# Kernel tuning notes

Measured on AMD Instinct MI355X. Metric: run time of the kernel, lower is better.

## Reference

```python
import jax, jax.numpy as jnp
import numpy as np

B, IN, OUT = 131072, 512, 512


def setup_inputs() -> dict:
    key = jax.random.key(0)
    k1, k2 = jax.random.split(key)
    x = jax.random.normal(k1, (B, IN), dtype=jnp.float32)
    # matches reset_parameters: normal(0, sqrt(1/in_features))
    weight = jax.random.normal(k2, (OUT, IN), dtype=jnp.float32) * jnp.sqrt(1.0 / IN)
    bias = jnp.zeros((OUT,), dtype=jnp.float32)
    return {"x": x, "weight": weight, "bias": bias}


def _binarize(w):
    # deterministic sign binarization: w >= 0 -> +1, else -1
    return jnp.where(w >= 0, 1.0, -1.0).astype(w.dtype)


def reference(x, weight, bias):
    wb = _binarize(weight)            # [out, in], values in {-1, +1}
    # out = x @ wb.T + bias           # [B, out]
    return jnp.einsum("bi,oi->bo", x, wb) + bias
```

## Files before the change

kernel.cpp:

```cpp
#include <hip/hip_runtime.h>
#include <stdint.h>


#define BATCH   131072
#define IN_F    512
#define OUT_F   512
#define BM      64
#define NCH     8
#define BUFB    16384

using f32x4  = __attribute__((ext_vector_type(4))) float;
using f32x16 = __attribute__((ext_vector_type(16))) float;
using short8 = __attribute__((ext_vector_type(8))) short;
using usv8   = __attribute__((ext_vector_type(8))) unsigned short;
using u32    = uint32_t;

__global__ void prep_w(const float* __restrict__ W, unsigned short* __restrict__ wf) {
    int t = blockIdx.x * blockDim.x + threadIdx.x;
    int l  = t & 63;
    int nf = (t >> 6) & 15;
    int kt = t >> 10;
    int n = nf * 32 + (l & 31);
    int k = kt * 16 + ((l >> 5) << 3);
    const float* src = W + (size_t)n * IN_F + k;
    f32x4 w0 = *(const f32x4*)(src);
    f32x4 w1 = *(const f32x4*)(src + 4);
    usv8 o;
#pragma unroll
    for (int j = 0; j < 4; ++j) {
        o[j]     = (w0[j] >= 0.0f) ? 0x3F80u : 0xBF80u;
        o[j + 4] = (w1[j] >= 0.0f) ? 0x3F80u : 0xBF80u;
    }
    *(usv8*)(wf + (size_t)t * 8) = o;
}

__global__ __launch_bounds__(512, 4) void gemm_bin(
    const float* __restrict__ X, const unsigned short* __restrict__ WF,
    const float* __restrict__ bias, float* __restrict__ out) {

    __shared__ __align__(16) char smem[4 * BUFB];

    const int tid  = threadIdx.x;
    const int lane = tid & 63;
    const int wv   = tid >> 6;
    const int m0   = blockIdx.x * BM;

    const int dr   = wv * 4 + (lane >> 4);
    const int ds4  = ((lane & 15) ^ (dr & 15)) << 2;
    const float* src0 = X + (size_t)(m0 + dr) * IN_F + ds4;
    const float* src1 = src0 + (size_t)32 * IN_F;

#define ISSUE_DMA(ck_)                                                         \
    {                                                                          \
        char* b_ = smem + ((ck_) & 3) * BUFB + wv * 1024;                      \
        __builtin_amdgcn_global_load_lds(                                      \
            (const __attribute__((address_space(1))) void*)(src0 + (ck_) * 64),\
            (__attribute__((address_space(3))) void*)(b_), 16, 0, 0);          \
        __builtin_amdgcn_global_load_lds(                                      \
            (const __attribute__((address_space(1))) void*)(src1 + (ck_) * 64),\
            (__attribute__((address_space(3))) void*)(b_ + 8192), 16, 0, 0);   \
    }

    const short8* wb = (const short8*)(WF) + ((size_t)(wv * 2) * 64 + lane);
#define LDB(dst, g_)                                                           \
    {                                                                          \
        _Pragma("unroll")                                                      \
        for (int fn = 0; fn < 2; ++fn)                                         \
            dst[fn] = wb[(g_) * 1024 + fn * 64];                               \
    }

    const int arow = (lane & 31) * 256;
    const int aq32 = (lane >> 5) << 5;
    const int aswz = (lane & 15) << 4;

#define LDA_CVT(dst, ab_, kt4_)                                                \
    {                                                                          \
        _Pragma("unroll")                                                      \
        for (int rg = 0; rg < 2; ++rg) {                                       \
            const char* p_  = (ab_) + rg * 8192 + arow;                        \
            const int  blo_ = (((kt4_) << 6) + aq32) ^ aswz;                   \
            f32x4 lo_ = *(const f32x4*)(p_ + blo_);                            \
            f32x4 hi_ = *(const f32x4*)(p_ + (blo_ ^ 16));                     \
            u32 w0_, w1_, w2_, w3_;                                            \
            asm("v_cvt_pk_bf16_f32 %0, %1, %2" : "=v"(w0_)                     \
                : "v"(lo_[0]), "v"(lo_[1]));                                   \
            asm("v_cvt_pk_bf16_f32 %0, %1, %2" : "=v"(w1_)                     \
                : "v"(lo_[2]), "v"(lo_[3]));                                   \
            asm("v_cvt_pk_bf16_f32 %0, %1, %2" : "=v"(w2_)                     \
                : "v"(hi_[0]), "v"(hi_[1]));                                   \
            asm("v_cvt_pk_bf16_f32 %0, %1, %2" : "=v"(w3_)                     \
                : "v"(hi_[2]), "v"(hi_[3]));                                   \
            union { u32 w[4]; short8 v; } pk_;                                 \
            pk_.w[0] = w0_; pk_.w[1] = w1_; pk_.w[2] = w2_; pk_.w[3] = w3_;    \
            dst[rg] = pk_.v;                                                   \
        }                                                                      \
    }

    f32x16 acc[2][2];
#pragma unroll
    for (int fn = 0; fn < 2; ++fn) {
        const float bv = bias[wv * 64 + fn * 32 + (lane & 31)];
#pragma unroll
        for (int rg = 0; rg < 2; ++rg)
#pragma unroll
            for (int r = 0; r < 16; ++r) acc[rg][fn][r] = bv;
    }

    ISSUE_DMA(0);
    ISSUE_DMA(1);

    short8 bf[2][2];
#pragma unroll
    for (int ck = 0; ck < NCH; ++ck) {
        LDB(bf[0], ck * 4 + 0);
        LDB(bf[1], ck * 4 + 1);
        __builtin_amdgcn_sched_barrier(0);
        if (ck < NCH - 1) asm volatile("s_waitcnt vmcnt(6)" ::: "memory");
        else              asm volatile("s_waitcnt vmcnt(4)" ::: "memory");
        __builtin_amdgcn_sched_barrier(0);
        __builtin_amdgcn_s_barrier();
        __builtin_amdgcn_sched_barrier(0);

        const char* ab = smem + (ck & 3) * BUFB;
        short8 af[2];
#pragma unroll
        for (int kt4 = 0; kt4 < 4; ++kt4) {
            LDA_CVT(af, ab, kt4);
            __builtin_amdgcn_s_setprio(1);
#pragma unroll
            for (int rg = 0; rg < 2; ++rg)
#pragma unroll
                for (int fn = 0; fn < 2; ++fn)
                    acc[rg][fn] = __builtin_amdgcn_mfma_f32_32x32x16_bf16(
                        af[rg], bf[kt4 & 1][fn], acc[rg][fn], 0, 0, 0);
            __builtin_amdgcn_s_setprio(0);
            if (kt4 < 2) LDB(bf[kt4 & 1], ck * 4 + kt4 + 2);
            if (kt4 == 1 && ck + 2 < NCH) {
                __builtin_amdgcn_sched_barrier(0);
                ISSUE_DMA(ck + 2);
                __builtin_amdgcn_sched_barrier(0);
            }
        }
    }
#undef ISSUE_DMA
#undef LDB
#undef LDA_CVT

    const int c     = lane & 31;
    const int rbase = (lane >> 5) << 2;
#pragma unroll
    for (int rg = 0; rg < 2; ++rg)
#pragma unroll
        for (int fn = 0; fn < 2; ++fn)
#pragma unroll
            for (int r = 0; r < 16; ++r) {
                const int row = rg * 32 + (r & 3) + 8 * (r >> 2) + rbase;
                out[(size_t)(m0 + row) * OUT_F + wv * 64 + fn * 32 + c] =
                    acc[rg][fn][r];
            }
}

extern "C" void kernel_launch(void* const* d_in, const int* in_sizes, int n_in,
                              void* d_out, int out_size, void* d_ws, size_t ws_size,
                              hipStream_t stream) {
    const float* X    = (const float*)d_in[0];
    const float* W    = (const float*)d_in[1];
    const float* bias = (const float*)d_in[2];
    float* o          = (float*)d_out;
    unsigned short* wf = (unsigned short*)d_ws;

    hipLaunchKernelGGL(prep_w, dim3(128), dim3(256), 0, stream, W, wf);
    hipLaunchKernelGGL(gemm_bin, dim3(BATCH / BM), dim3(512), 0, stream,
                       X, wf, bias, o);
}
```

Measured before the change: 138.8 us.

## Pack binarized weights into sign bits and split output columns across XCD-mapped blocks

```diff
diff --git a/kernel.cpp b/kernel.cpp
--- a/kernel.cpp
+++ b/kernel.cpp
@@ -5,37 +5,51 @@
 #define BATCH   131072
 #define IN_F    512
 #define OUT_F   512
-#define BM      64
+#define BM      32
 #define NCH     8
-#define BUFB    16384
+#define BUFB    8192
 
 using f32x4  = __attribute__((ext_vector_type(4))) float;
 using f32x16 = __attribute__((ext_vector_type(16))) float;
 using short8 = __attribute__((ext_vector_type(8))) short;
-using usv8   = __attribute__((ext_vector_type(8))) unsigned short;
 using u32    = uint32_t;
+using u64    = unsigned long long;
 
-__global__ void prep_w(const float* __restrict__ W, unsigned short* __restrict__ wf) {
+__global__ void prep_wbits(const float* __restrict__ W, u32* __restrict__ wp) {
     int t = blockIdx.x * blockDim.x + threadIdx.x;
     int l  = t & 63;
-    int nf = (t >> 6) & 15;
-    int kt = t >> 10;
-    int n = nf * 32 + (l & 31);
-    int k = kt * 16 + ((l >> 5) << 3);
-    const float* src = W + (size_t)n * IN_F + k;
-    f32x4 w0 = *(const f32x4*)(src);
-    f32x4 w1 = *(const f32x4*)(src + 4);
-    usv8 o;
+    int nf = t >> 6;
+    const float* row = W + (size_t)(nf * 32 + (l & 31)) * IN_F + ((l >> 5) << 3);
 #pragma unroll
-    for (int j = 0; j < 4; ++j) {
-        o[j]     = (w0[j] >= 0.0f) ? 0x3F80u : 0xBF80u;
-        o[j + 4] = (w1[j] >= 0.0f) ? 0x3F80u : 0xBF80u;
+    for (int q = 0; q < 8; ++q) {
+        u32 word = 0;
+#pragma unroll
+        for (int b = 0; b < 4; ++b) {
+            const float* p = row + (q * 4 + b) * 16;
+            u32 by = 0;
+#pragma unroll
+            for (int j = 0; j < 8; ++j)
+                by |= (p[j] >= 0.0f ? 0u : 1u) << j;
+            word |= by << (8 * b);
+        }
+        wp[(size_t)t * 8 + q] = word;
     }
-    *(usv8*)(wf + (size_t)t * 8) = o;
 }
 
-__global__ __launch_bounds__(512, 4) void gemm_bin(
-    const float* __restrict__ X, const unsigned short* __restrict__ WF,
+__device__ __forceinline__ short8 expB(u32 bb) {
+    const u64 MUL = 0x1000200040008000ull;
+    const u64 MSK = 0x8000800080008000ull;
+    const u64 ONE = 0x3F803F803F803F80ull;
+    u64 lo = ((u64)(bb & 0xFu) * MUL) & MSK;
+    u64 hi = ((u64)((bb >> 4) & 0xFu) * MUL) & MSK;
+    union { u64 d[2]; short8 v; } pk;
+    pk.d[0] = ONE | lo;
+    pk.d[1] = ONE | hi;
+    return pk.v;
+}
+
+__global__ __launch_bounds__(256, 4) void gemm_bin(
+    const float* __restrict__ X, const u32* __restrict__ WP,
     const float* __restrict__ bias, float* __restrict__ out) {
 
     __shared__ __align__(16) char smem[4 * BUFB];
@@ -43,12 +57,19 @@
     const int tid  = threadIdx.x;
     const int lane = tid & 63;
     const int wv   = tid >> 6;
-    const int m0   = blockIdx.x * BM;
+
+    const int d     = blockIdx.x;
+    const int xcd   = d & 7;
+    const int i     = d >> 3;
+    const int q     = i & 1;
+    const int strip = (i >> 1) * 8 + xcd;
+    const int m0    = strip * BM;
+    const int col0  = q * 256 + wv * 64;
 
     const int dr   = wv * 4 + (lane >> 4);
     const int ds4  = ((lane & 15) ^ (dr & 15)) << 2;
     const float* src0 = X + (size_t)(m0 + dr) * IN_F + ds4;
-    const float* src1 = src0 + (size_t)32 * IN_F;
+    const float* src1 = src0 + (size_t)16 * IN_F;
 
 #define ISSUE_DMA(ck_)                                                         \
     {                                                                          \
@@ -58,106 +79,84 @@
             (__attribute__((address_space(3))) void*)(b_), 16, 0, 0);          \
         __builtin_amdgcn_global_load_lds(                                      \
             (const __attribute__((address_space(1))) void*)(src1 + (ck_) * 64),\
-            (__attribute__((address_space(3))) void*)(b_ + 8192), 16, 0, 0);   \
+            (__attribute__((address_space(3))) void*)(b_ + 4096), 16, 0, 0);   \
     }
 
-    const short8* wb = (const short8*)(WF) + ((size_t)(wv * 2) * 64 + lane);
-#define LDB(dst, g_)                                                           \
-    {                                                                          \
-        _Pragma("unroll")                                                      \
-        for (int fn = 0; fn < 2; ++fn)                                         \
-            dst[fn] = wb[(g_) * 1024 + fn * 64];                               \
-    }
+    const u32* wpp = WP + (((size_t)(q * 8 + wv * 2) * 64 + lane) << 3);
+    uint4 a0 = *(const uint4*)(wpp);
+    uint4 a1 = *(const uint4*)(wpp + 4);
+    uint4 b0 = *(const uint4*)(wpp + 512);
+    uint4 b1 = *(const uint4*)(wpp + 516);
+    __builtin_amdgcn_sched_barrier(0);
+
+    ISSUE_DMA(0);
+    ISSUE_DMA(1);
+    ISSUE_DMA(2);
+    __builtin_amdgcn_sched_barrier(0);
+
+    const u32 w0[8] = {a0.x, a0.y, a0.z, a0.w, a1.x, a1.y, a1.z, a1.w};
+    const u32 w1[8] = {b0.x, b0.y, b0.z, b0.w, b1.x, b1.y, b1.z, b1.w};
 
     const int arow = (lane & 31) * 256;
     const int aq32 = (lane >> 5) << 5;
     const int aswz = (lane & 15) << 4;
 
-#define LDA_CVT(dst, ab_, kt4_)                                                \
-    {                                                                          \
-        _Pragma("unroll")                                                      \
-        for (int rg = 0; rg < 2; ++rg) {                                       \
-            const char* p_  = (ab_) + rg * 8192 + arow;                        \
-            const int  blo_ = (((kt4_) << 6) + aq32) ^ aswz;                   \
-            f32x4 lo_ = *(const f32x4*)(p_ + blo_);                            \
-            f32x4 hi_ = *(const f32x4*)(p_ + (blo_ ^ 16));                     \
-            u32 w0_, w1_, w2_, w3_;                                            \
-            asm("v_cvt_pk_bf16_f32 %0, %1, %2" : "=v"(w0_)                     \
-                : "v"(lo_[0]), "v"(lo_[1]));                                   \
-            asm("v_cvt_pk_bf16_f32 %0, %1, %2" : "=v"(w1_)                     \
-                : "v"(lo_[2]), "v"(lo_[3]));                                   \
-            asm("v_cvt_pk_bf16_f32 %0, %1, %2" : "=v"(w2_)                     \
-                : "v"(hi_[0]), "v"(hi_[1]));                                   \
-            asm("v_cvt_pk_bf16_f32 %0, %1, %2" : "=v"(w3_)                     \
-                : "v"(hi_[2]), "v"(hi_[3]));                                   \
-            union { u32 w[4]; short8 v; } pk_;                                 \
-            pk_.w[0] = w0_; pk_.w[1] = w1_; pk_.w[2] = w2_; pk_.w[3] = w3_;    \
-            dst[rg] = pk_.v;                                                   \
-        }                                                                      \
+    f32x16 acc[2];
+#pragma unroll
+    for (int fn = 0; fn < 2; ++fn) {
+        const float bv = bias[col0 + fn * 32 + (lane & 31)];
+#pragma unroll
+        for (int r = 0; r < 16; ++r) acc[fn][r] = bv;
     }
 
-    f32x16 acc[2][2];
-#pragma unroll
-    for (int fn = 0; fn < 2; ++fn) {
-        const float bv = bias[wv * 64 + fn * 32 + (lane & 31)];
-#pragma unroll
-        for (int rg = 0; rg < 2; ++rg)
-#pragma unroll
-            for (int r = 0; r < 16; ++r) acc[rg][fn][r] = bv;
-    }
-
-    ISSUE_DMA(0);
-    ISSUE_DMA(1);
-
-    short8 bf[2][2];
 #pragma unroll
     for (int ck = 0; ck < NCH; ++ck) {
-        LDB(bf[0], ck * 4 + 0);
-        LDB(bf[1], ck * 4 + 1);
+        short8 bf[4][2];
+#pragma unroll
+        for (int k4 = 0; k4 < 4; ++k4) {
+            const int kt = ck * 4 + k4;
+            bf[k4][0] = expB(w0[kt >> 2] >> ((kt & 3) * 8));
+            bf[k4][1] = expB(w1[kt >> 2] >> ((kt & 3) * 8));
+        }
         __builtin_amdgcn_sched_barrier(0);
-        if (ck < NCH - 1) asm volatile("s_waitcnt vmcnt(6)" ::: "memory");
-        else              asm volatile("s_waitcnt vmcnt(4)" ::: "memory");
+        if (ck < NCH - 2)       asm volatile("s_waitcnt vmcnt(4)" ::: "memory");
+        else if (ck == NCH - 2) asm volatile("s_waitcnt vmcnt(2)" ::: "memory");
+        else                    asm volatile("s_waitcnt vmcnt(0)" ::: "memory");
         __builtin_amdgcn_sched_barrier(0);
         __builtin_amdgcn_s_barrier();
         __builtin_amdgcn_sched_barrier(0);
+        if (ck + 3 < NCH) ISSUE_DMA(ck + 3);
 
         const char* ab = smem + (ck & 3) * BUFB;
-        short8 af[2];
 #pragma unroll
-        for (int kt4 = 0; kt4 < 4; ++kt4) {
-            LDA_CVT(af, ab, kt4);
+        for (int k4 = 0; k4 < 4; ++k4) {
+            const int blo = ((k4 << 6) + aq32) ^ aswz;
+            f32x4 lo = *(const f32x4*)(ab + arow + blo);
+            f32x4 hi = *(const f32x4*)(ab + arow + (blo ^ 16));
+            u32 c0, c1, c2, c3;
+            asm("v_cvt_pk_bf16_f32 %0, %1, %2" : "=v"(c0) : "v"(lo[0]), "v"(lo[1]));
+            asm("v_cvt_pk_bf16_f32 %0, %1, %2" : "=v"(c1) : "v"(lo[2]), "v"(lo[3]));
+            asm("v_cvt_pk_bf16_f32 %0, %1, %2" : "=v"(c2) : "v"(hi[0]), "v"(hi[1]));
+            asm("v_cvt_pk_bf16_f32 %0, %1, %2" : "=v"(c3) : "v"(hi[2]), "v"(hi[3]));
+            union { u32 w[4]; short8 v; } pk;
+            pk.w[0] = c0; pk.w[1] = c1; pk.w[2] = c2; pk.w[3] = c3;
             __builtin_amdgcn_s_setprio(1);
-#pragma unroll
-            for (int rg = 0; rg < 2; ++rg)
-#pragma unroll
-                for (int fn = 0; fn < 2; ++fn)
-                    acc[rg][fn] = __builtin_amdgcn_mfma_f32_32x32x16_bf16(
-                        af[rg], bf[kt4 & 1][fn], acc[rg][fn], 0, 0, 0);
+            acc[0] = __builtin_amdgcn_mfma_f32_32x32x16_bf16(pk.v, bf[k4][0], acc[0], 0, 0, 0);
+            acc[1] = __builtin_amdgcn_mfma_f32_32x32x16_bf16(pk.v, bf[k4][1], acc[1], 0, 0, 0);
             __builtin_amdgcn_s_setprio(0);
-            if (kt4 < 2) LDB(bf[kt4 & 1], ck * 4 + kt4 + 2);
-            if (kt4 == 1 && ck + 2 < NCH) {
-                __builtin_amdgcn_sched_barrier(0);
-                ISSUE_DMA(ck + 2);
-                __builtin_amdgcn_sched_barrier(0);
-            }
         }
     }
 #undef ISSUE_DMA
-#undef LDB
-#undef LDA_CVT
 
     const int c     = lane & 31;
     const int rbase = (lane >> 5) << 2;
 #pragma unroll
-    for (int rg = 0; rg < 2; ++rg)
+    for (int fn = 0; fn < 2; ++fn)
 #pragma unroll
-        for (int fn = 0; fn < 2; ++fn)
-#pragma unroll
-            for (int r = 0; r < 16; ++r) {
-                const int row = rg * 32 + (r & 3) + 8 * (r >> 2) + rbase;
-                out[(size_t)(m0 + row) * OUT_F + wv * 64 + fn * 32 + c] =
-                    acc[rg][fn][r];
-            }
+        for (int r = 0; r < 16; ++r) {
+            const int row = (r & 3) + 8 * (r >> 2) + rbase;
+            out[(size_t)(m0 + row) * OUT_F + col0 + fn * 32 + c] = acc[fn][r];
+        }
 }
 
 extern "C" void kernel_launch(void* const* d_in, const int* in_sizes, int n_in,
@@ -167,9 +166,9 @@
     const float* W    = (const float*)d_in[1];
     const float* bias = (const float*)d_in[2];
     float* o          = (float*)d_out;
-    unsigned short* wf = (unsigned short*)d_ws;
+    u32* wp           = (u32*)d_ws;
 
-    hipLaunchKernelGGL(prep_w, dim3(128), dim3(256), 0, stream, W, wf);
-    hipLaunchKernelGGL(gemm_bin, dim3(BATCH / BM), dim3(512), 0, stream,
-                       X, wf, bias, o);
+    hipLaunchKernelGGL(prep_wbits, dim3(4), dim3(256), 0, stream, W, wp);
+    hipLaunchKernelGGL(gemm_bin, dim3(2 * BATCH / BM), dim3(256), 0, stream,
+                       X, wp, bias, o);
 }
```

Measured after the change: 128.3 us. -7.6%, faster.
